# Performance work log

Measured on AMD Instinct MI355X. Metric: run time of the kernel, lower is better.

## Reference

```python
import jax, jax.numpy as jnp
import numpy as np

ND, NP_, NC, H, L, B = 4000, 19000, 1000, 128, 2, 30000
E_DP, E_PP, E_CP = 200000, 300000, 150000


def setup_inputs() -> dict:
    key = jax.random.key(0)
    ks = iter(jax.random.split(key, 64))
    def nrm(shape, s=0.05):
        return jax.random.normal(next(ks), shape, dtype=jnp.float32) * s
    inp = {
        'drug_emb': nrm((ND, H)), 'protein_emb': nrm((NP_, H)), 'cell_emb': nrm((NC, H)),
    }
    for r in ['dp', 'rdp', 'pp', 'cp', 'rcp']:
        inp['W_' + r] = nrm((L, H, H))
        inp['a_src_' + r] = nrm((L, H))
        inp['a_dst_' + r] = nrm((L, H))
        inp['b_' + r] = jnp.zeros((L, H), jnp.float32)
    inp['W1'] = nrm((3 * H, 6 * H)); inp['b1'] = jnp.zeros((6 * H,), jnp.float32)
    inp['W2'] = nrm((6 * H, 2 * H)); inp['b2'] = jnp.zeros((2 * H,), jnp.float32)
    inp['W3'] = nrm((2 * H, 2)); inp['b3'] = jnp.zeros((2,), jnp.float32)
    def ri(n, hi):
        return jax.random.randint(next(ks), (n,), 0, hi, dtype=jnp.int32)
    inp['src_dp'] = ri(E_DP, ND); inp['dst_dp'] = ri(E_DP, NP_)
    inp['src_pp'] = ri(E_PP, NP_); inp['dst_pp'] = ri(E_PP, NP_)
    inp['src_cp'] = ri(E_CP, NC); inp['dst_cp'] = ri(E_CP, NP_)
    inp['drug1'] = ri(B, ND); inp['drug2'] = ri(B, ND); inp['cell'] = ri(B, NC)
    return inp


def _gat(x_src, x_dst, W, a_s, a_d, b, src, dst, n_dst):
    # Single-head PyG GATConv: shared linear, additive attention, segment softmax over dst.
    h_s = x_src @ W                      # [Ns, H]
    h_d = x_dst @ W                      # [Nd, H]
    e = jax.nn.leaky_relu((h_s @ a_s)[src] + (h_d @ a_d)[dst], 0.2)  # [E]
    m = jax.lax.stop_gradient(jax.ops.segment_max(e, dst, num_segments=n_dst))
    p = jnp.exp(e - m[dst])
    denom = jax.ops.segment_sum(p, dst, num_segments=n_dst)
    alpha = p / denom[dst]
    out = jax.ops.segment_sum(alpha[:, None] * h_s[src], dst, num_segments=n_dst)
    return out + b


def _l2norm(x):
    return x / jnp.maximum(jnp.linalg.norm(x, axis=1, keepdims=True), 1e-12)


def reference(drug_emb, protein_emb, cell_emb,
              W_dp, a_src_dp, a_dst_dp, b_dp,
              W_rdp, a_src_rdp, a_dst_rdp, b_rdp,
              W_pp, a_src_pp, a_dst_pp, b_pp,
              W_cp, a_src_cp, a_dst_cp, b_cp,
              W_rcp, a_src_rcp, a_dst_rcp, b_rcp,
              W1, b1, W2, b2, W3, b3,
              src_dp, dst_dp, src_pp, dst_pp, src_cp, dst_cp,
              drug1, drug2, cell):
    # p-p uses add_self_loops=True
    loops = jnp.arange(NP_, dtype=src_pp.dtype)
    spp = jnp.concatenate([src_pp, loops]); dpp = jnp.concatenate([dst_pp, loops])
    x_d, x_p, x_c = drug_emb, protein_emb, cell_emb
    for l in range(L):
        out_p = _gat(x_d, x_p, W_dp[l], a_src_dp[l], a_dst_dp[l], b_dp[l], src_dp, dst_dp, NP_)
        out_p = out_p + _gat(x_p, x_p, W_pp[l], a_src_pp[l], a_dst_pp[l], b_pp[l], spp, dpp, NP_)
        out_p = out_p + _gat(x_c, x_p, W_cp[l], a_src_cp[l], a_dst_cp[l], b_cp[l], src_cp, dst_cp, NP_)
        out_d = _gat(x_p, x_d, W_rdp[l], a_src_rdp[l], a_dst_rdp[l], b_rdp[l], dst_dp, src_dp, ND)
        out_c = _gat(x_p, x_c, W_rcp[l], a_src_rcp[l], a_dst_rcp[l], b_rcp[l], dst_cp, src_cp, NC)
        x_d, x_p, x_c = jax.nn.relu(out_d), jax.nn.relu(out_p), jax.nn.relu(out_c)
    hid = jnp.concatenate([_l2norm(x_d[drug1]), _l2norm(x_d[drug2]), _l2norm(x_c[cell])], axis=1)
    h = jax.nn.relu(hid @ W1 + b1)
    h = jax.nn.relu(h @ W2 + b2)
    return h @ W3 + b3
```

## Files before the change

kernel.cpp:

```cpp
#include <hip/hip_runtime.h>
#include <hip/hip_bf16.h>

#define H 128
#define ND 4000
#define NPN 19000
#define NCN 1000
#define NLAYERS 2
#define NB 30000
#define E_DP 200000
#define E_PP 300000
#define E_CP 150000

typedef __bf16 bf16_t;
typedef bf16_t bf16x8 __attribute__((ext_vector_type(8)));
typedef float f32x4 __attribute__((ext_vector_type(4)));
typedef unsigned short u16;

static __device__ __forceinline__ float wred_sum(float v) {
#pragma unroll
  for (int off = 32; off; off >>= 1) v += __shfl_xor(v, off);
  return v;
}
static __device__ __forceinline__ float bflo(unsigned u) { return __uint_as_float(u << 16); }
static __device__ __forceinline__ float bfhi(unsigned u) { return __uint_as_float(u & 0xffff0000u); }
static __device__ __forceinline__ unsigned packbf(float v0, float v1) {
  union { bf16_t b; unsigned short u; } a, b;
  a.b = (bf16_t)v0; b.b = (bf16_t)v1;
  return (unsigned)a.u | ((unsigned)b.u << 16);
}

#define GLDS16(gp, lp) \
  __builtin_amdgcn_global_load_lds((__attribute__((address_space(1))) void*)(gp), \
                                   (__attribute__((address_space(3))) void*)(lp), 16, 0, 0)

__device__ __forceinline__ void mfma_core(
    const bf16_t* __restrict__ A, const bf16_t* __restrict__ Bt,
    int M, int K, int ldb, int m0, int n0, f32x4 (&acc)[4][4])
{
  __shared__ char As[128 * 64];
  __shared__ char Bs[128 * 64];
  const int t = threadIdx.x;
  const int lane = t & 63;
#pragma unroll
  for (int mi = 0; mi < 4; ++mi)
#pragma unroll
    for (int ni = 0; ni < 4; ++ni) acc[mi][ni] = (f32x4){0.f, 0.f, 0.f, 0.f};

  const int wid = t >> 6;
  const int wr = wid >> 1, wc = wid & 1;
  const int sr = t >> 2;
  const int sc = t & 3;
  const int csrc = ((sc ^ ((sr >> 1) & 3)) << 4);
  int ra0 = m0 + sr;      if (ra0 >= M) ra0 = M - 1;
  int ra1 = m0 + 64 + sr; if (ra1 >= M) ra1 = M - 1;
  const char* gA0 = (const char*)A + (size_t)ra0 * K * 2 + csrc;
  const char* gA1 = (const char*)A + (size_t)ra1 * K * 2 + csrc;
  const char* gB0 = (const char*)Bt + (size_t)(n0 + sr) * ldb * 2 + csrc;
  const char* gB1 = (const char*)Bt + (size_t)(n0 + 64 + sr) * ldb * 2 + csrc;
  char* lA0 = As + t * 16;
  char* lA1 = As + 4096 + t * 16;
  char* lB0 = Bs + t * 16;
  char* lB1 = Bs + 4096 + t * 16;

  int aoff[4], boff[4];
#pragma unroll
  for (int mi = 0; mi < 4; ++mi) {
    int r = wr * 64 + mi * 16 + (lane & 15);
    aoff[mi] = r * 64 + ((((lane >> 4)) ^ ((r >> 1) & 3)) << 4);
  }
#pragma unroll
  for (int ni = 0; ni < 4; ++ni) {
    int r = wc * 64 + ni * 16 + (lane & 15);
    boff[ni] = r * 64 + ((((lane >> 4)) ^ ((r >> 1) & 3)) << 4);
  }

  for (int k0 = 0; k0 < K; k0 += 32) {
    const size_t kb = (size_t)k0 * 2;
    __syncthreads();
    GLDS16(gA0 + kb, lA0);
    GLDS16(gA1 + kb, lA1);
    GLDS16(gB0 + kb, lB0);
    GLDS16(gB1 + kb, lB1);
    __syncthreads();
    bf16x8 av[4], bv[4];
#pragma unroll
    for (int mi = 0; mi < 4; ++mi) av[mi] = *(const bf16x8*)(As + aoff[mi]);
#pragma unroll
    for (int ni = 0; ni < 4; ++ni) bv[ni] = *(const bf16x8*)(Bs + boff[ni]);
#pragma unroll
    for (int mi = 0; mi < 4; ++mi)
#pragma unroll
      for (int ni = 0; ni < 4; ++ni)
        acc[mi][ni] = __builtin_amdgcn_mfma_f32_16x16x32_bf16(av[mi], bv[ni], acc[mi][ni], 0, 0, 0);
  }
}

struct GJob { const bf16_t* A; const bf16_t* Bt; bf16_t* C; int M; int K;
              const float *b1, *b2, *b3; };
struct Gemm3 { GJob j[3]; };
__global__ __launch_bounds__(256) void k_gemm_g3(Gemm3 g) {
  const GJob& jb = g.j[blockIdx.y];
  int m0 = blockIdx.x * 128;
  if (m0 >= jb.M) return;
  f32x4 acc[4][4];
  mfma_core(jb.A, jb.Bt, jb.M, jb.K, jb.K, m0, 0, acc);
  const int t = threadIdx.x, lane = t & 63, wid = t >> 6;
  const int wr = wid >> 1, wc = wid & 1;
  const int col0 = lane & 15, rsub = (lane >> 4) * 4;
#pragma unroll
  for (int mi = 0; mi < 4; ++mi) {
#pragma unroll
    for (int ni = 0; ni < 4; ++ni) {
      int c = wc * 64 + ni * 16 + col0;
      float bb = jb.b1[c];
      if (jb.b2) bb += jb.b2[c];
      if (jb.b3) bb += jb.b3[c];
#pragma unroll
      for (int rg = 0; rg < 4; ++rg) {
        int r = m0 + wr * 64 + mi * 16 + rsub + rg;
        if (r < jb.M) jb.C[(size_t)r * H + c] = (bf16_t)fmaxf(acc[mi][ni][rg] + bb, 0.f);
      }
    }
  }
}

struct PJob { const bf16_t* A; float* C; int M; const float* rs; };
struct GemmPS { PJob j[3]; const bf16_t* Bt; };
__global__ __launch_bounds__(256) void k_gemm_ps(GemmPS g) {
  const PJob& jb = g.j[blockIdx.y];
  int mt = blockIdx.x / 6, nt = blockIdx.x - mt * 6;
  int m0 = mt * 128;
  if (m0 >= jb.M) return;
  int n0 = nt * 128;
  f32x4 acc[4][4];
  mfma_core(jb.A, g.Bt + blockIdx.y * 128, jb.M, 128, 384, m0, n0, acc);
  const int t = threadIdx.x, lane = t & 63, wid = t >> 6;
  const int wr = wid >> 1, wc = wid & 1;
  const int col0 = lane & 15, rsub = (lane >> 4) * 4;
#pragma unroll
  for (int mi = 0; mi < 4; ++mi) {
#pragma unroll
    for (int rg = 0; rg < 4; ++rg) {
      int r = m0 + wr * 64 + mi * 16 + rsub + rg;
      if (r < jb.M) {
        float sc = jb.rs[r];
#pragma unroll
        for (int ni = 0; ni < 4; ++ni) {
          int c = n0 + wc * 64 + ni * 16 + col0;
          jb.C[(size_t)r * 768 + c] = acc[mi][ni][rg] * sc;
        }
      }
    }
  }
}

__global__ __launch_bounds__(256) void k_gemm_w2o(
    const bf16_t* __restrict__ h1, const bf16_t* __restrict__ W2t,
    const float* __restrict__ b2, const float* __restrict__ W3, const float* __restrict__ b3,
    float* __restrict__ out, int cn, int c0)
{
  int m0 = blockIdx.x * 128;
  int n0 = blockIdx.y * 128;
  if (m0 >= cn) return;
  f32x4 acc[4][4];
  mfma_core(h1, W2t, cn, 768, 768, m0, n0, acc);
  const int t = threadIdx.x, lane = t & 63, wid = t >> 6;
  const int wr = wid >> 1, wc = wid & 1;
  const int col0 = lane & 15, rsub = (lane >> 4) * 4;
  float w0[4], w1[4], bb[4];
#pragma unroll
  for (int ni = 0; ni < 4; ++ni) {
    int c = n0 + wc * 64 + ni * 16 + col0;
    w0[ni] = W3[2 * c]; w1[ni] = W3[2 * c + 1]; bb[ni] = b2[c];
  }
  const int addb = (n0 == 0 && wc == 0);
#pragma unroll
  for (int mi = 0; mi < 4; ++mi) {
#pragma unroll
    for (int rg = 0; rg < 4; ++rg) {
      int r = m0 + wr * 64 + mi * 16 + rsub + rg;
      float p0 = 0.f, p1 = 0.f;
#pragma unroll
      for (int ni = 0; ni < 4; ++ni) {
        float v = fmaxf(acc[mi][ni][rg] + bb[ni], 0.f);
        p0 = fmaf(v, w0[ni], p0);
        p1 = fmaf(v, w1[ni], p1);
      }
#pragma unroll
      for (int off = 1; off < 16; off <<= 1) {
        p0 += __shfl_xor(p0, off);
        p1 += __shfl_xor(p1, off);
      }
      if (col0 == 0 && r < cn) {
        if (addb) { p0 += b3[0]; p1 += b3[1]; }
        atomicAdd(&out[(size_t)(c0 + r) * 2], p0);
        atomicAdd(&out[(size_t)(c0 + r) * 2 + 1], p1);
      }
    }
  }
}

__global__ __launch_bounds__(256) void k_conv_emb(
    const float* __restrict__ xd, const float* __restrict__ xp, const float* __restrict__ xc,
    bf16_t* __restrict__ od, bf16_t* __restrict__ op, bf16_t* __restrict__ oc)
{
  int i = blockIdx.x * 256 + threadIdx.x;
  const int SD = ND * H, SP = NPN * H, SC = NCN * H;
  if (i < SD) od[i] = (bf16_t)xd[i];
  else if (i < SD + SP) op[i - SD] = (bf16_t)xp[i - SD];
  else if (i < SD + SP + SC) oc[i - SD - SP] = (bf16_t)xc[i - SD - SP];
}

struct TC { const float* src[12]; bf16_t* dst[12]; int Ksub[12]; int N[12]; int Kfull[12]; int koff[12]; };
__global__ __launch_bounds__(256) void k_tconv2(TC a) {
  int m = blockIdx.z;
  int Ks = a.Ksub[m], N = a.N[m];
  int tx = blockIdx.x * 32;
  int ty = blockIdx.y * 32;
  if (tx >= N || ty >= Ks) return;
  __shared__ float tile[32][33];
  int c = threadIdx.x & 31, rr = threadIdx.x >> 5;
#pragma unroll
  for (int kk = rr; kk < 32; kk += 8)
    if (ty + kk < Ks && tx + c < N) tile[kk][c] = a.src[m][(size_t)(ty + kk) * N + tx + c];
  __syncthreads();
  bf16_t* dst = a.dst[m];
  int Kf = a.Kfull[m], ko = a.koff[m];
#pragma unroll
  for (int nn = rr; nn < 32; nn += 8)
    if (tx + nn < N && ty + c < Ks)
      dst[(size_t)(tx + nn) * Kf + ko + ty + c] = (bf16_t)tile[c][nn];
}

struct Wd20 { const float* W[20]; const float* a[20]; float* o[20]; };
__global__ __launch_bounds__(128) void k_wd20(Wd20 g) {
  int m = blockIdx.x;
  int k = threadIdx.x;
  const float* Wp = g.W[m];
  const float* av = g.a[m];
  float s = 0.f;
#pragma unroll 4
  for (int j = 0; j < H; ++j) s = fmaf(Wp[k * H + j], av[j], s);
  g.o[m][k] = s;
}

struct Sc { const bf16_t* xd; const bf16_t* xp; const bf16_t* xc; const float* wv;
            float* ss[5]; float* sd[5]; };
__global__ __launch_bounds__(256) void k_scores(Sc S) {
  int row = blockIdx.x * 4 + (threadIdx.x >> 6);
  if (row >= ND + NPN + NCN) return;
  int lane = threadIdx.x & 63;
  const bf16_t* x;
  int idx, cls;
  if (row < ND) { x = S.xd; idx = row; cls = 0; }
  else if (row < ND + NPN) { x = S.xp; idx = row - ND; cls = 1; }
  else { x = S.xc; idx = row - ND - NPN; cls = 2; }
  unsigned u = *(const unsigned*)(x + (size_t)idx * H + lane * 2);
  float x0 = bflo(u), x1 = bfhi(u);
  const float* wv = S.wv;
#define DOT(vi, outp) { const float* v = wv + (vi) * H; \
    float s = x0 * v[2 * lane] + x1 * v[2 * lane + 1]; s = wred_sum(s); \
    if (!lane) (outp)[idx] = s; }
  if (cls == 0) {
    DOT(0, S.ss[0]); DOT(8, S.sd[3]);
  } else if (cls == 1) {
    DOT(1, S.ss[1]); DOT(3, S.ss[3]); DOT(4, S.ss[4]);
    DOT(5, S.sd[0]); DOT(6, S.sd[1]); DOT(7, S.sd[2]);
  } else {
    DOT(2, S.ss[2]); DOT(9, S.sd[4]);
  }
#undef DOT
}

struct CsrArgs {
  const int* src[5]; const int* dst[5];
  int E[5]; int n[5];
  int* cnt[5]; int* cur[5]; int* starts[5]; u16* csr[5];
};
__global__ __launch_bounds__(256) void k_count5(CsrArgs a) {
  int rel = blockIdx.y;
  int e = blockIdx.x * 256 + threadIdx.x;
  if (e >= a.E[rel]) return;
  atomicAdd(&a.cnt[rel][a.dst[rel][e]], 1);
}
__global__ __launch_bounds__(1024) void k_scan5(CsrArgs a) {
  int rel = blockIdx.x;
  int n = a.n[rel];
  const int* cnt = a.cnt[rel];
  int* st = a.starts[rel];
  int* cu = a.cur[rel];
  int t = threadIdx.x;
  int stripe = (n + 1023) / 1024;
  int lo = t * stripe;
  int hi = lo + stripe; if (hi > n) hi = n;
  int s = 0;
  for (int i = lo; i < hi; ++i) s += cnt[i];
  int lane = t & 63, wv = t >> 6;
  int x = s;
#pragma unroll
  for (int off = 1; off < 64; off <<= 1) {
    int y = __shfl_up(x, off);
    if (lane >= off) x += y;
  }
  __shared__ int ws[16];
  if (lane == 63) ws[wv] = x;
  __syncthreads();
  if (t == 0) {
    int run = 0;
#pragma unroll
    for (int i = 0; i < 16; ++i) { int v = ws[i]; ws[i] = run; run += v; }
  }
  __syncthreads();
  int run = ws[wv] + x - s;
  for (int i = lo; i < hi; ++i) { st[i] = run; cu[i] = run; run += cnt[i]; }
  if (t == 1023) st[n] = ws[15] + x;
}
__global__ __launch_bounds__(256) void k_fill5(CsrArgs a) {
  int rel = blockIdx.y;
  int e = blockIdx.x * 256 + threadIdx.x;
  if (e >= a.E[rel]) return;
  int d = a.dst[rel][e];
  int s = a.src[rel][e];
  int pos = atomicAdd(&a.cur[rel][d], 1);
  a.csr[rel][pos] = (u16)s;
}

struct Agg5 {
  const u16* csr[5]; const int* starts[5];
  const float* ss[5]; const float* sd[5];
  const bf16_t* xs[5];
  bf16_t* y[5]; int ystride[5]; int ycoff[5]; int ndst[5]; int self[5];
};
__global__ __launch_bounds__(256) void k_agg5(Agg5 a) {
  int rel = blockIdx.y;
  int d = blockIdx.x * 4 + (threadIdx.x >> 6);
  if (d >= a.ndst[rel]) return;
  int lane = threadIdx.x & 63;
  int g = lane >> 4, j16 = lane & 15;
  bf16_t* yrow = a.y[rel] + (size_t)d * a.ystride[rel] + a.ycoff[rel];
  int s0 = a.starts[rel][d];
  int deg = a.starts[rel][d + 1] - s0;
  int selfa = a.self[rel];
  if (!deg && !selfa) {
    if (g == 0) *(uint4*)(yrow + j16 * 8) = make_uint4(0u, 0u, 0u, 0u);
    return;
  }
  const u16* cs = a.csr[rel] + s0;
  const float* ssp = a.ss[rel];
  const bf16_t* xsp = a.xs[rel];
  float sdv = a.sd[rel][d];
  float acc[8] = {0.f, 0.f, 0.f, 0.f, 0.f, 0.f, 0.f, 0.f};
  float ps = 0.f;
  for (int b = 0; b < deg; b += 16) {
#pragma unroll
    for (int u = 0; u < 4; ++u) {
      int i = b + u * 4 + g;
      float p = 0.f;
      uint4 U = make_uint4(0u, 0u, 0u, 0u);
      if (i < deg) {
        int s = cs[i];
        float e = ssp[s] + sdv; e = e > 0.f ? e : 0.2f * e;
        p = __expf(e);
        U = *(const uint4*)(xsp + (size_t)s * H + j16 * 8);
      }
      ps += p;
      acc[0] = fmaf(p, bflo(U.x), acc[0]); acc[1] = fmaf(p, bfhi(U.x), acc[1]);
      acc[2] = fmaf(p, bflo(U.y), acc[2]); acc[3] = fmaf(p, bfhi(U.y), acc[3]);
      acc[4] = fmaf(p, bflo(U.z), acc[4]); acc[5] = fmaf(p, bfhi(U.z), acc[5]);
      acc[6] = fmaf(p, bflo(U.w), acc[6]); acc[7] = fmaf(p, bfhi(U.w), acc[7]);
    }
  }
  if (selfa && g == 0) {
    float e = ssp[d] + sdv; e = e > 0.f ? e : 0.2f * e;
    float p = __expf(e);
    uint4 U = *(const uint4*)(xsp + (size_t)d * H + j16 * 8);
    ps += p;
    acc[0] = fmaf(p, bflo(U.x), acc[0]); acc[1] = fmaf(p, bfhi(U.x), acc[1]);
    acc[2] = fmaf(p, bflo(U.y), acc[2]); acc[3] = fmaf(p, bfhi(U.y), acc[3]);
    acc[4] = fmaf(p, bflo(U.z), acc[4]); acc[5] = fmaf(p, bfhi(U.z), acc[5]);
    acc[6] = fmaf(p, bflo(U.w), acc[6]); acc[7] = fmaf(p, bfhi(U.w), acc[7]);
  }
#pragma unroll
  for (int e = 0; e < 8; ++e) {
    acc[e] += __shfl_xor(acc[e], 16);
    acc[e] += __shfl_xor(acc[e], 32);
  }
  ps += __shfl_xor(ps, 16);
  ps += __shfl_xor(ps, 32);
  if (g == 0) {
    float inv = 1.f / ps;
    uint4 O;
    O.x = packbf(acc[0] * inv, acc[1] * inv);
    O.y = packbf(acc[2] * inv, acc[3] * inv);
    O.z = packbf(acc[4] * inv, acc[5] * inv);
    O.w = packbf(acc[6] * inv, acc[7] * inv);
    *(uint4*)(yrow + j16 * 8) = O;
  }
}

__global__ __launch_bounds__(256) void k_invnorm(
    const bf16_t* __restrict__ xd, const bf16_t* __restrict__ xc,
    float* __restrict__ invd, float* __restrict__ invc)
{
  int row = blockIdx.x * 4 + (threadIdx.x >> 6);
  if (row >= ND + NCN) return;
  int lane = threadIdx.x & 63;
  const bf16_t* x = (row < ND) ? xd + (size_t)row * H : xc + (size_t)(row - ND) * H;
  unsigned u = ((const unsigned*)x)[lane];
  float av = bflo(u), bv = bfhi(u);
  float s = wred_sum(av * av + bv * bv);
  if (!lane) {
    float nv = fmaxf(sqrtf(s), 1e-12f);
    if (row < ND) invd[row] = 1.f / nv; else invc[row - ND] = 1.f / nv;
  }
}

__global__ __launch_bounds__(256) void k_pairsum(
    const float* __restrict__ Pa, const float* __restrict__ Pb, const float* __restrict__ Pc,
    const float* __restrict__ b1,
    const int* __restrict__ d1, const int* __restrict__ d2, const int* __restrict__ ce,
    bf16_t* __restrict__ h1, int c0, int cn)
{
  int gid = blockIdx.x * 256 + threadIdx.x;
  if (gid >= cn * 96) return;
  int i = gid / 96, c = gid - i * 96;
  int gi = c0 + i;
  int ra = d1[gi], rb = d2[gi], rc = ce[gi];
  const float4* pa = (const float4*)(Pa + (size_t)ra * 768 + c * 8);
  const float4* pb = (const float4*)(Pb + (size_t)rb * 768 + c * 8);
  const float4* pc = (const float4*)(Pc + (size_t)rc * 768 + c * 8);
  const float4* bb = (const float4*)(b1 + c * 8);
  float4 s0 = pa[0], s1 = pa[1];
  float4 t0 = pb[0], t1 = pb[1];
  float4 u0 = pc[0], u1 = pc[1];
  float4 v0 = bb[0], v1 = bb[1];
  uint4 O;
  O.x = packbf(fmaxf(s0.x + t0.x + u0.x + v0.x, 0.f), fmaxf(s0.y + t0.y + u0.y + v0.y, 0.f));
  O.y = packbf(fmaxf(s0.z + t0.z + u0.z + v0.z, 0.f), fmaxf(s0.w + t0.w + u0.w + v0.w, 0.f));
  O.z = packbf(fmaxf(s1.x + t1.x + u1.x + v1.x, 0.f), fmaxf(s1.y + t1.y + u1.y + v1.y, 0.f));
  O.w = packbf(fmaxf(s1.z + t1.z + u1.z + v1.z, 0.f), fmaxf(s1.w + t1.w + u1.w + v1.w, 0.f));
  *(uint4*)(h1 + (size_t)i * 768 + c * 8) = O;
}

extern "C" void kernel_launch(void* const* d_in, const int* in_sizes, int n_in,
                              void* d_out, int out_size, void* d_ws, size_t ws_size,
                              hipStream_t stream)
{
  (void)in_sizes; (void)n_in;
  const float* drug_emb    = (const float*)d_in[0];
  const float* protein_emb = (const float*)d_in[1];
  const float* cell_emb    = (const float*)d_in[2];
  const int base_idx[5] = {3, 11, 15, 7, 19};
  const float *W_[5], *as_[5], *ad_[5], *b_[5];
  for (int r = 0; r < 5; ++r) {
    W_[r]  = (const float*)d_in[base_idx[r]];
    as_[r] = (const float*)d_in[base_idx[r] + 1];
    ad_[r] = (const float*)d_in[base_idx[r] + 2];
    b_[r]  = (const float*)d_in[base_idx[r] + 3];
  }
  const float* W1 = (const float*)d_in[23]; const float* b1 = (const float*)d_in[24];
  const float* W2 = (const float*)d_in[25]; const float* b2 = (const float*)d_in[26];
  const float* W3 = (const float*)d_in[27]; const float* b3 = (const float*)d_in[28];
  const int* src_dp = (const int*)d_in[29]; const int* dst_dp = (const int*)d_in[30];
  const int* src_pp = (const int*)d_in[31]; const int* dst_pp = (const int*)d_in[32];
  const int* src_cp = (const int*)d_in[33]; const int* dst_cp = (const int*)d_in[34];
  const int* drug1  = (const int*)d_in[35]; const int* drug2  = (const int*)d_in[36];
  const int* cellb  = (const int*)d_in[37];
  float* out = (float*)d_out;

  char* wsb = (char*)d_ws;
  size_t off = 0;
  auto alloc = [&](size_t bytes) -> void* {
    void* p = wsb + off;
    off += (bytes + 255) & ~(size_t)255;
    return p;
  };
  bf16_t* xdb[2] = {(bf16_t*)alloc((size_t)ND * H * 2),  (bf16_t*)alloc((size_t)ND * H * 2)};
  bf16_t* xpb[2] = {(bf16_t*)alloc((size_t)NPN * H * 2), (bf16_t*)alloc((size_t)NPN * H * 2)};
  bf16_t* xcb[2] = {(bf16_t*)alloc((size_t)NCN * H * 2), (bf16_t*)alloc((size_t)NCN * H * 2)};
  const int Msrc[5] = {ND, NPN, NCN, NPN, NPN};
  const int Mdst[5] = {NPN, NPN, NPN, ND, NCN};
  const int Erel[5] = {E_DP, E_PP, E_CP, E_DP, E_CP};
  bf16_t* yp = (bf16_t*)alloc((size_t)NPN * 384 * 2);
  bf16_t* yd = (bf16_t*)alloc((size_t)ND * H * 2);
  bf16_t* yc = (bf16_t*)alloc((size_t)NCN * H * 2);
  bf16_t* Wtp = (bf16_t*)alloc((size_t)NLAYERS * 128 * 384 * 2);
  bf16_t* Wtd = (bf16_t*)alloc((size_t)NLAYERS * 128 * 128 * 2);
  bf16_t* Wtc = (bf16_t*)alloc((size_t)NLAYERS * 128 * 128 * 2);
  bf16_t* W1t = (bf16_t*)alloc((size_t)768 * 384 * 2);
  bf16_t* W2t = (bf16_t*)alloc((size_t)256 * 768 * 2);
  float* wvb = (float*)alloc(20 * H * 4);
  float* ssb[5]; for (int r = 0; r < 5; ++r) ssb[r] = (float*)alloc((size_t)Msrc[r] * 4);
  float* sdb[5]; for (int r = 0; r < 5; ++r) sdb[r] = (float*)alloc((size_t)Mdst[r] * 4);
  int* cnt_all = (int*)alloc(62000 * 4);
  int* cur_all = (int*)alloc(62000 * 4);
  int* st_all  = (int*)alloc((62000 + 5) * 4);
  int *cntb[5], *curb[5], *stb[5];
  { int o = 0, o2 = 0;
    for (int r = 0; r < 5; ++r) {
      cntb[r] = cnt_all + o; curb[r] = cur_all + o; stb[r] = st_all + o2;
      o += Mdst[r]; o2 += Mdst[r] + 1;
    } }
  u16* csrb[5]; for (int r = 0; r < 5; ++r) csrb[r] = (u16*)alloc((size_t)Erel[r] * 2);
  float* invd = (float*)alloc(ND * 4);
  float* invc = (float*)alloc(NCN * 4);
  float* P1a = (float*)alloc((size_t)ND * 768 * 4);
  float* P1b = (float*)alloc((size_t)ND * 768 * 4);
  float* P1c = (float*)alloc((size_t)NCN * 768 * 4);
  size_t fixed_end = off;
  size_t avail = ws_size > fixed_end ? ws_size - fixed_end : 0;
  long long cmax = (long long)avail / 1536;
  int CH = cmax > NB ? NB : (int)cmax;
  CH &= ~255;
  if (CH < 256) CH = 256;
  bf16_t* h1 = (bf16_t*)alloc((size_t)CH * 768 * 2);

  hipMemsetAsync(out, 0, (size_t)out_size * 4, stream);

  k_conv_emb<<<(ND * H + NPN * H + NCN * H + 255) / 256, 256, 0, stream>>>(
      drug_emb, protein_emb, cell_emb, xdb[0], xpb[0], xcb[0]);
  TC tc;
  for (int l = 0; l < 2; ++l) {
    for (int r = 0; r < 3; ++r) {
      int m = l * 3 + r;
      tc.src[m] = W_[r] + (size_t)l * H * H;
      tc.dst[m] = Wtp + (size_t)l * 128 * 384;
      tc.Ksub[m] = 128; tc.N[m] = 128; tc.Kfull[m] = 384; tc.koff[m] = r * 128;
    }
    tc.src[6 + l] = W_[3] + (size_t)l * H * H; tc.dst[6 + l] = Wtd + (size_t)l * 128 * 128;
    tc.Ksub[6 + l] = 128; tc.N[6 + l] = 128; tc.Kfull[6 + l] = 128; tc.koff[6 + l] = 0;
    tc.src[8 + l] = W_[4] + (size_t)l * H * H; tc.dst[8 + l] = Wtc + (size_t)l * 128 * 128;
    tc.Ksub[8 + l] = 128; tc.N[8 + l] = 128; tc.Kfull[8 + l] = 128; tc.koff[8 + l] = 0;
  }
  tc.src[10] = W1; tc.dst[10] = W1t; tc.Ksub[10] = 384; tc.N[10] = 768; tc.Kfull[10] = 384; tc.koff[10] = 0;
  tc.src[11] = W2; tc.dst[11] = W2t; tc.Ksub[11] = 768; tc.N[11] = 256; tc.Kfull[11] = 768; tc.koff[11] = 0;
  k_tconv2<<<dim3(24, 24, 12), 256, 0, stream>>>(tc);

  Wd20 wg;
  for (int l = 0; l < 2; ++l)
    for (int r = 0; r < 5; ++r) {
      int m = l * 10 + r;
      wg.W[m] = W_[r] + (size_t)l * H * H; wg.a[m] = as_[r] + l * H; wg.o[m] = wvb + m * H;
      int m2 = l * 10 + 5 + r;
      wg.W[m2] = W_[r] + (size_t)l * H * H; wg.a[m2] = ad_[r] + l * H; wg.o[m2] = wvb + m2 * H;
    }
  k_wd20<<<20, 128, 0, stream>>>(wg);

  hipMemsetAsync(cnt_all, 0, 62000 * 4, stream);
  CsrArgs ca;
  const int* srcA[5] = {src_dp, src_pp, src_cp, dst_dp, dst_cp};
  const int* dstA[5] = {dst_dp, dst_pp, dst_cp, src_dp, src_cp};
  for (int r = 0; r < 5; ++r) {
    ca.src[r] = srcA[r]; ca.dst[r] = dstA[r]; ca.E[r] = Erel[r]; ca.n[r] = Mdst[r];
    ca.cnt[r] = cntb[r]; ca.cur[r] = curb[r]; ca.starts[r] = stb[r]; ca.csr[r] = csrb[r];
  }
  dim3 egrid((E_PP + 255) / 256, 5);
  k_count5<<<egrid, 256, 0, stream>>>(ca);
  k_scan5<<<5, 1024, 0, stream>>>(ca);
  k_fill5<<<egrid, 256, 0, stream>>>(ca);

  int cur = 0;
  for (int l = 0; l < NLAYERS; ++l) {
    int nxt = 1 - cur;
    const bf16_t* xsrc[5] = {xdb[cur], xpb[cur], xcb[cur], xpb[cur], xpb[cur]};
    Sc sc;
    sc.xd = xdb[cur]; sc.xp = xpb[cur]; sc.xc = xcb[cur]; sc.wv = wvb + l * 10 * H;
    for (int r = 0; r < 5; ++r) { sc.ss[r] = ssb[r]; sc.sd[r] = sdb[r]; }
    k_scores<<<(ND + NPN + NCN + 3) / 4, 256, 0, stream>>>(sc);
    Agg5 aa;
    bf16_t* yptr[5] = {yp, yp, yp, yd, yc};
    const int ystr[5] = {384, 384, 384, 128, 128};
    const int ycof[5] = {0, 128, 256, 0, 0};
    const int selfs[5] = {0, 1, 0, 0, 0};
    for (int r = 0; r < 5; ++r) {
      aa.csr[r] = csrb[r]; aa.starts[r] = stb[r]; aa.ss[r] = ssb[r]; aa.sd[r] = sdb[r];
      aa.xs[r] = xsrc[r]; aa.y[r] = yptr[r]; aa.ystride[r] = ystr[r]; aa.ycoff[r] = ycof[r];
      aa.ndst[r] = Mdst[r]; aa.self[r] = selfs[r];
    }
    k_agg5<<<dim3((NPN + 3) / 4, 5), 256, 0, stream>>>(aa);
    Gemm3 g3;
    g3.j[0] = {yp, Wtp + (size_t)l * 128 * 384, xpb[nxt], NPN, 384,
               b_[0] + l * H, b_[1] + l * H, b_[2] + l * H};
    g3.j[1] = {yd, Wtd + (size_t)l * 128 * 128, xdb[nxt], ND, 128,
               b_[3] + l * H, nullptr, nullptr};
    g3.j[2] = {yc, Wtc + (size_t)l * 128 * 128, xcb[nxt], NCN, 128,
               b_[4] + l * H, nullptr, nullptr};
    k_gemm_g3<<<dim3((NPN + 127) / 128, 3), 256, 0, stream>>>(g3);
    cur = nxt;
  }

  k_invnorm<<<(ND + NCN + 3) / 4, 256, 0, stream>>>(xdb[cur], xcb[cur], invd, invc);
  GemmPS ps;
  ps.Bt = W1t;
  ps.j[0] = {xdb[cur], P1a, ND, invd};
  ps.j[1] = {xdb[cur], P1b, ND, invd};
  ps.j[2] = {xcb[cur], P1c, NCN, invc};
  k_gemm_ps<<<dim3(32 * 6, 3), 256, 0, stream>>>(ps);
  for (int c0 = 0; c0 < NB; c0 += CH) {
    int cn = (NB - c0 < CH) ? (NB - c0) : CH;
    k_pairsum<<<((size_t)cn * 96 + 255) / 256, 256, 0, stream>>>(
        P1a, P1b, P1c, b1, drug1, drug2, cellb, h1, c0, cn);
    k_gemm_w2o<<<dim3((cn + 127) / 128, 2), 256, 0, stream>>>(
        h1, W2t, b2, W3, b3, out, cn, c0);
  }
}
```

Before: 443.1 us.

## Fuse pairwise gather-sum into W2 GEMM head and batch CSR build threads

The pairsum kernel that gathered three projected rows, added bias, applied ReLU and wrote a bf16 h1 buffer is removed. The W2 GEMM head now does that work itself while staging its A operand into shared memory. This drops the 30000x768 intermediate write and re-read and the chunked launch loop, but each of the two column blocks repeats the fp32 gathers. Separately, the CSR count and fill kernels now process four edges per thread with a quarter of the blocks.

```diff
diff --git a/kernel.cpp b/kernel.cpp
--- a/kernel.cpp
+++ b/kernel.cpp
@@ -154,18 +154,95 @@
   }
 }
 
-__global__ __launch_bounds__(256) void k_gemm_w2o(
-    const bf16_t* __restrict__ h1, const bf16_t* __restrict__ W2t,
-    const float* __restrict__ b2, const float* __restrict__ W3, const float* __restrict__ b3,
-    float* __restrict__ out, int cn, int c0)
+__global__ __launch_bounds__(256) void k_w2head(
+    const float* __restrict__ Pa, const float* __restrict__ Pb, const float* __restrict__ Pc,
+    const float* __restrict__ b1,
+    const int* __restrict__ d1, const int* __restrict__ d2, const int* __restrict__ ce,
+    const bf16_t* __restrict__ W2t, const float* __restrict__ b2,
+    const float* __restrict__ W3, const float* __restrict__ b3,
+    float* __restrict__ out, int cn)
 {
-  int m0 = blockIdx.x * 128;
-  int n0 = blockIdx.y * 128;
+  __shared__ char As[128 * 64];
+  __shared__ char Bs[128 * 64];
+  const int t = threadIdx.x;
+  const int lane = t & 63;
+  const int m0 = blockIdx.x * 128;
+  const int n0 = blockIdx.y * 128;
   if (m0 >= cn) return;
   f32x4 acc[4][4];
-  mfma_core(h1, W2t, cn, 768, 768, m0, n0, acc);
-  const int t = threadIdx.x, lane = t & 63, wid = t >> 6;
+#pragma unroll
+  for (int mi = 0; mi < 4; ++mi)
+#pragma unroll
+    for (int ni = 0; ni < 4; ++ni) acc[mi][ni] = (f32x4){0.f, 0.f, 0.f, 0.f};
+
+  const int arow = t >> 1;
+  const int ah = t & 1;
+  int gr = m0 + arow; if (gr >= cn) gr = cn - 1;
+  const float* pa = Pa + (size_t)d1[gr] * 768 + ah * 16;
+  const float* pb = Pb + (size_t)d2[gr] * 768 + ah * 16;
+  const float* pc = Pc + (size_t)ce[gr] * 768 + ah * 16;
+  const int swz = (arow >> 1) & 3;
+  char* la0 = As + arow * 64 + (((ah * 2)     ^ swz) << 4);
+  char* la1 = As + arow * 64 + (((ah * 2 + 1) ^ swz) << 4);
+
+  const int sr = t >> 2;
+  const int sc = t & 3;
+  const int csrc = ((sc ^ ((sr >> 1) & 3)) << 4);
+  const char* gB0 = (const char*)W2t + (size_t)(n0 + sr) * 768 * 2 + csrc;
+  const char* gB1 = (const char*)W2t + (size_t)(n0 + 64 + sr) * 768 * 2 + csrc;
+  char* lB0 = Bs + t * 16;
+  char* lB1 = Bs + 4096 + t * 16;
+
+  const int wid = t >> 6;
   const int wr = wid >> 1, wc = wid & 1;
+  int aoff[4], boff[4];
+#pragma unroll
+  for (int mi = 0; mi < 4; ++mi) {
+    int r = wr * 64 + mi * 16 + (lane & 15);
+    aoff[mi] = r * 64 + ((((lane >> 4)) ^ ((r >> 1) & 3)) << 4);
+  }
+#pragma unroll
+  for (int ni = 0; ni < 4; ++ni) {
+    int r = wc * 64 + ni * 16 + (lane & 15);
+    boff[ni] = r * 64 + ((((lane >> 4)) ^ ((r >> 1) & 3)) << 4);
+  }
+
+  for (int k0 = 0; k0 < 768; k0 += 32) {
+    const float4* qa = (const float4*)(pa + k0);
+    const float4* qb = (const float4*)(pb + k0);
+    const float4* qc = (const float4*)(pc + k0);
+    const float4* qb1 = (const float4*)(b1 + k0 + ah * 16);
+    float4 A0 = qa[0], A1 = qa[1], A2 = qa[2], A3 = qa[3];
+    float4 B0 = qb[0], B1 = qb[1], B2 = qb[2], B3 = qb[3];
+    float4 C0 = qc[0], C1 = qc[1], C2 = qc[2], C3 = qc[3];
+    float4 D0 = qb1[0], D1 = qb1[1], D2 = qb1[2], D3 = qb1[3];
+    uint4 P0, P1;
+    P0.x = packbf(fmaxf(A0.x + B0.x + C0.x + D0.x, 0.f), fmaxf(A0.y + B0.y + C0.y + D0.y, 0.f));
+    P0.y = packbf(fmaxf(A0.z + B0.z + C0.z + D0.z, 0.f), fmaxf(A0.w + B0.w + C0.w + D0.w, 0.f));
+    P0.z = packbf(fmaxf(A1.x + B1.x + C1.x + D1.x, 0.f), fmaxf(A1.y + B1.y + C1.y + D1.y, 0.f));
+    P0.w = packbf(fmaxf(A1.z + B1.z + C1.z + D1.z, 0.f), fmaxf(A1.w + B1.w + C1.w + D1.w, 0.f));
+    P1.x = packbf(fmaxf(A2.x + B2.x + C2.x + D2.x, 0.f), fmaxf(A2.y + B2.y + C2.y + D2.y, 0.f));
+    P1.y = packbf(fmaxf(A2.z + B2.z + C2.z + D2.z, 0.f), fmaxf(A2.w + B2.w + C2.w + D2.w, 0.f));
+    P1.z = packbf(fmaxf(A3.x + B3.x + C3.x + D3.x, 0.f), fmaxf(A3.y + B3.y + C3.y + D3.y, 0.f));
+    P1.w = packbf(fmaxf(A3.z + B3.z + C3.z + D3.z, 0.f), fmaxf(A3.w + B3.w + C3.w + D3.w, 0.f));
+    __syncthreads();
+    GLDS16(gB0 + (size_t)k0 * 2, lB0);
+    GLDS16(gB1 + (size_t)k0 * 2, lB1);
+    *(uint4*)la0 = P0;
+    *(uint4*)la1 = P1;
+    __syncthreads();
+    bf16x8 av[4], bv[4];
+#pragma unroll
+    for (int mi = 0; mi < 4; ++mi) av[mi] = *(const bf16x8*)(As + aoff[mi]);
+#pragma unroll
+    for (int ni = 0; ni < 4; ++ni) bv[ni] = *(const bf16x8*)(Bs + boff[ni]);
+#pragma unroll
+    for (int mi = 0; mi < 4; ++mi)
+#pragma unroll
+      for (int ni = 0; ni < 4; ++ni)
+        acc[mi][ni] = __builtin_amdgcn_mfma_f32_16x16x32_bf16(av[mi], bv[ni], acc[mi][ni], 0, 0, 0);
+  }
+
   const int col0 = lane & 15, rsub = (lane >> 4) * 4;
   float w0[4], w1[4], bb[4];
 #pragma unroll
@@ -193,8 +270,8 @@
       }
       if (col0 == 0 && r < cn) {
         if (addb) { p0 += b3[0]; p1 += b3[1]; }
-        atomicAdd(&out[(size_t)(c0 + r) * 2], p0);
-        atomicAdd(&out[(size_t)(c0 + r) * 2 + 1], p1);
+        atomicAdd(&out[(size_t)r * 2], p0);
+        atomicAdd(&out[(size_t)r * 2 + 1], p1);
       }
     }
   }
@@ -279,9 +356,15 @@
 };
 __global__ __launch_bounds__(256) void k_count5(CsrArgs a) {
   int rel = blockIdx.y;
-  int e = blockIdx.x * 256 + threadIdx.x;
-  if (e >= a.E[rel]) return;
-  atomicAdd(&a.cnt[rel][a.dst[rel][e]], 1);
+  int E = a.E[rel];
+  const int* dst = a.dst[rel];
+  int* cnt = a.cnt[rel];
+  int e0 = blockIdx.x * 1024 + threadIdx.x;
+#pragma unroll
+  for (int u = 0; u < 4; ++u) {
+    int e = e0 + u * 256;
+    if (e < E) atomicAdd(&cnt[dst[e]], 1);
+  }
 }
 __global__ __launch_bounds__(1024) void k_scan5(CsrArgs a) {
   int rel = blockIdx.x;
@@ -317,12 +400,20 @@
 }
 __global__ __launch_bounds__(256) void k_fill5(CsrArgs a) {
   int rel = blockIdx.y;
-  int e = blockIdx.x * 256 + threadIdx.x;
-  if (e >= a.E[rel]) return;
-  int d = a.dst[rel][e];
-  int s = a.src[rel][e];
-  int pos = atomicAdd(&a.cur[rel][d], 1);
-  a.csr[rel][pos] = (u16)s;
+  int E = a.E[rel];
+  const int* dst = a.dst[rel];
+  const int* src = a.src[rel];
+  int* cur = a.cur[rel];
+  u16* csr = a.csr[rel];
+  int e0 = blockIdx.x * 1024 + threadIdx.x;
+#pragma unroll
+  for (int u = 0; u < 4; ++u) {
+    int e = e0 + u * 256;
+    if (e < E) {
+      int pos = atomicAdd(&cur[dst[e]], 1);
+      csr[pos] = (u16)src[e];
+    }
+  }
 }
 
 struct Agg5 {
@@ -413,33 +504,6 @@
     float nv = fmaxf(sqrtf(s), 1e-12f);
     if (row < ND) invd[row] = 1.f / nv; else invc[row - ND] = 1.f / nv;
   }
-}
-
-__global__ __launch_bounds__(256) void k_pairsum(
-    const float* __restrict__ Pa, const float* __restrict__ Pb, const float* __restrict__ Pc,
-    const float* __restrict__ b1,
-    const int* __restrict__ d1, const int* __restrict__ d2, const int* __restrict__ ce,
-    bf16_t* __restrict__ h1, int c0, int cn)
-{
-  int gid = blockIdx.x * 256 + threadIdx.x;
-  if (gid >= cn * 96) return;
-  int i = gid / 96, c = gid - i * 96;
-  int gi = c0 + i;
-  int ra = d1[gi], rb = d2[gi], rc = ce[gi];
-  const float4* pa = (const float4*)(Pa + (size_t)ra * 768 + c * 8);
-  const float4* pb = (const float4*)(Pb + (size_t)rb * 768 + c * 8);
-  const float4* pc = (const float4*)(Pc + (size_t)rc * 768 + c * 8);
-  const float4* bb = (const float4*)(b1 + c * 8);
-  float4 s0 = pa[0], s1 = pa[1];
-  float4 t0 = pb[0], t1 = pb[1];
-  float4 u0 = pc[0], u1 = pc[1];
-  float4 v0 = bb[0], v1 = bb[1];
-  uint4 O;
-  O.x = packbf(fmaxf(s0.x + t0.x + u0.x + v0.x, 0.f), fmaxf(s0.y + t0.y + u0.y + v0.y, 0.f));
-  O.y = packbf(fmaxf(s0.z + t0.z + u0.z + v0.z, 0.f), fmaxf(s0.w + t0.w + u0.w + v0.w, 0.f));
-  O.z = packbf(fmaxf(s1.x + t1.x + u1.x + v1.x, 0.f), fmaxf(s1.y + t1.y + u1.y + v1.y, 0.f));
-  O.w = packbf(fmaxf(s1.z + t1.z + u1.z + v1.z, 0.f), fmaxf(s1.w + t1.w + u1.w + v1.w, 0.f));
-  *(uint4*)(h1 + (size_t)i * 768 + c * 8) = O;
 }
 
 extern "C" void kernel_launch(void* const* d_in, const int* in_sizes, int n_in,
@@ -507,13 +571,7 @@
   float* P1a = (float*)alloc((size_t)ND * 768 * 4);
   float* P1b = (float*)alloc((size_t)ND * 768 * 4);
   float* P1c = (float*)alloc((size_t)NCN * 768 * 4);
-  size_t fixed_end = off;
-  size_t avail = ws_size > fixed_end ? ws_size - fixed_end : 0;
-  long long cmax = (long long)avail / 1536;
-  int CH = cmax > NB ? NB : (int)cmax;
-  CH &= ~255;
-  if (CH < 256) CH = 256;
-  bf16_t* h1 = (bf16_t*)alloc((size_t)CH * 768 * 2);
+  (void)ws_size;
 
   hipMemsetAsync(out, 0, (size_t)out_size * 4, stream);
 
@@ -554,7 +612,7 @@
     ca.src[r] = srcA[r]; ca.dst[r] = dstA[r]; ca.E[r] = Erel[r]; ca.n[r] = Mdst[r];
     ca.cnt[r] = cntb[r]; ca.cur[r] = curb[r]; ca.starts[r] = stb[r]; ca.csr[r] = csrb[r];
   }
-  dim3 egrid((E_PP + 255) / 256, 5);
+  dim3 egrid((E_PP + 1023) / 1024, 5);
   k_count5<<<egrid, 256, 0, stream>>>(ca);
   k_scan5<<<5, 1024, 0, stream>>>(ca);
   k_fill5<<<egrid, 256, 0, stream>>>(ca);
@@ -596,11 +654,6 @@
   ps.j[1] = {xdb[cur], P1b, ND, invd};
   ps.j[2] = {xcb[cur], P1c, NCN, invc};
   k_gemm_ps<<<dim3(32 * 6, 3), 256, 0, stream>>>(ps);
-  for (int c0 = 0; c0 < NB; c0 += CH) {
-    int cn = (NB - c0 < CH) ? (NB - c0) : CH;
-    k_pairsum<<<((size_t)cn * 96 + 255) / 256, 256, 0, stream>>>(
-        P1a, P1b, P1c, b1, drug1, drug2, cellb, h1, c0, cn);
-    k_gemm_w2o<<<dim3((cn + 127) / 128, 2), 256, 0, stream>>>(
-        h1, W2t, b2, W3, b3, out, cn, c0);
-  }
-}
+  k_w2head<<<dim3((NB + 127) / 128, 2), 256, 0, stream>>>(
+      P1a, P1b, P1c, b1, drug1, drug2, cellb, W2t, b2, W3, b3, out, NB);
+}
```

After: 418.3 us. -5.6%, faster.
